# Performance work log

Hardware: AMD Instinct MI355X
Metric: run time of the kernel (lower is better)

The kernel has to match this reference:

```python
import jax, jax.numpy as jnp
import numpy as np

T, B, OBS, HID = 64, 1024, 8, 512
N_ODE_STEPS = 4  # fixed-step RK4 over t in [0, 1]
LN_EPS = 1e-5


def _ln(x, g, b):
    m = x.mean(-1, keepdims=True)
    v = ((x - m) ** 2).mean(-1, keepdims=True)
    return (x - m) / jnp.sqrt(v + LN_EPS) * g + b


def setup_inputs() -> dict:
    key = jax.random.key(0)
    ks = jax.random.split(key, 24)

    def w(k, shape, fan_in):
        s = 1.0 / np.sqrt(fan_in)
        return jax.random.uniform(k, shape, jnp.float32, -s, s)

    return {
        "xs": jax.random.normal(ks[0], (T, B, OBS), jnp.float32),
        # obs2hidden MLP: Linear + LayerNorm + LeakyReLU
        "obs_W": w(ks[1], (OBS, HID), OBS),
        "obs_b": w(ks[2], (HID,), OBS),
        "obs_ln_g": jnp.ones((HID,), jnp.float32),
        "obs_ln_b": jnp.zeros((HID,), jnp.float32),
        # ODE func MLP (time-concat input, 2 hidden layers, linear out)
        "ode_W1": w(ks[3], (HID + 1, HID), HID + 1),
        "ode_b1": w(ks[4], (HID,), HID + 1),
        "ode_ln1_g": jnp.ones((HID,), jnp.float32),
        "ode_ln1_b": jnp.zeros((HID,), jnp.float32),
        "ode_W2": w(ks[5], (HID, HID), HID),
        "ode_b2": w(ks[6], (HID,), HID),
        "ode_ln2_g": jnp.ones((HID,), jnp.float32),
        "ode_ln2_b": jnp.zeros((HID,), jnp.float32),
        "ode_Wout": w(ks[7], (HID, HID), HID),
        "ode_bout": w(ks[8], (HID,), HID),
        # GRU cell (torch gate order: r, z, n)
        "W_ih": w(ks[9], (HID, 3 * HID), HID),
        "b_ih": w(ks[10], (3 * HID,), HID),
        "W_hh": w(ks[11], (HID, 3 * HID), HID),
        "b_hh": w(ks[12], (3 * HID,), HID),
    }


def reference(xs, obs_W, obs_b, obs_ln_g, obs_ln_b,
              ode_W1, ode_b1, ode_ln1_g, ode_ln1_b,
              ode_W2, ode_b2, ode_ln2_g, ode_ln2_b,
              ode_Wout, ode_bout, W_ih, b_ih, W_hh, b_hh):
    batch = xs.shape[1]

    # obs -> hidden for all timesteps at once: [T, B, HID]
    hs = jax.nn.leaky_relu(_ln(xs @ obs_W + obs_b, obs_ln_g, obs_ln_b))

    def ode_f(h, t):  # h: [B, HID], t: scalar
        ht = jnp.concatenate([h, jnp.full((batch, 1), t, h.dtype)], axis=-1)
        z = jax.nn.leaky_relu(_ln(ht @ ode_W1 + ode_b1, ode_ln1_g, ode_ln1_b))
        z = jax.nn.leaky_relu(_ln(z @ ode_W2 + ode_b2, ode_ln2_g, ode_ln2_b))
        return z @ ode_Wout + ode_bout

    dt = 1.0 / N_ODE_STEPS

    def rk4_solve(h0):
        def body(h, t):
            k1 = ode_f(h, t)
            k2 = ode_f(h + 0.5 * dt * k1, t + 0.5 * dt)
            k3 = ode_f(h + 0.5 * dt * k2, t + 0.5 * dt)
            k4 = ode_f(h + dt * k3, t + dt)
            return h + (dt / 6.0) * (k1 + 2 * k2 + 2 * k3 + k4), None
        ts = jnp.arange(N_ODE_STEPS, dtype=h0.dtype) * dt
        h, _ = jax.lax.scan(body, h0, ts)
        return h

    def gru_cell(x, h):
        gi = x @ W_ih + b_ih
        gh = h @ W_hh + b_hh
        i_r, i_z, i_n = jnp.split(gi, 3, axis=-1)
        h_r, h_z, h_n = jnp.split(gh, 3, axis=-1)
        r = jax.nn.sigmoid(i_r + h_r)
        z = jax.nn.sigmoid(i_z + h_z)
        n = jnp.tanh(i_n + r * h_n)
        return (1.0 - z) * n + z * h

    def step(h_prev, h_obs):
        h_ode = rk4_solve(h_obs)          # NeuralODE: integrate from t=0 to 1
        h_new = gru_cell(h_ode, h_prev)   # GRU step
        return h_new, None

    h0 = jnp.zeros((batch, hs.shape[-1]), hs.dtype)
    h_final, _ = jax.lax.scan(step, h0, hs)
    return h_final  # [B, HID]
```

## Files before the change

kernel.cpp:

```cpp
#include <hip/hip_runtime.h>
#include <stdint.h>


typedef __bf16 bf16x8 __attribute__((ext_vector_type(8)));
typedef float floatx4 __attribute__((ext_vector_type(4)));

#define BP 40
#define KSP 516

static __device__ __forceinline__ float bf2f(unsigned short u) {
  union { unsigned int u32; float f; } c;
  c.u32 = ((unsigned int)u) << 16;
  return c.f;
}
static __device__ __forceinline__ unsigned short f2bf(float f) {
  union { __bf16 h; unsigned short u; } c;
  c.h = (__bf16)f;
  return c.u;
}
static __device__ __forceinline__ float lo_bf(unsigned int u) {
  union { unsigned int i; float f; } c; c.i = u << 16; return c.f;
}
static __device__ __forceinline__ float hi_bf(unsigned int u) {
  union { unsigned int i; float f; } c; c.i = u & 0xffff0000u; return c.f;
}
static __device__ __forceinline__ unsigned int pk2(float a, float b) {
  return (unsigned int)f2bf(a) | ((unsigned int)f2bf(b) << 16);
}

static __device__ __forceinline__ void barrier_lds() {
  __asm__ volatile("s_waitcnt lgkmcnt(0)\n\ts_barrier" ::: "memory");
}

static __device__ __forceinline__ float row16_sum(float v) {
  union { float f; int i; } c, d;
  c.f = v;
  d.i = __builtin_amdgcn_update_dpp(0, c.i, 0x111, 0xf, 0xf, true); c.f += d.f;
  d.i = __builtin_amdgcn_update_dpp(0, c.i, 0x112, 0xf, 0xf, true); c.f += d.f;
  d.i = __builtin_amdgcn_update_dpp(0, c.i, 0x114, 0xf, 0xf, true); c.f += d.f;
  d.i = __builtin_amdgcn_update_dpp(0, c.i, 0x118, 0xf, 0xf, true); c.f += d.f;
  return c.f;
}

__global__ void tile_weight(const float* __restrict__ src, unsigned short* __restrict__ dst) {
  int t = blockIdx.x * 256 + threadIdx.x;
  int ml = t & 15, qd = (t >> 4) & 3;
  int nt = (t >> 6) & 31, kk = t >> 11;
  int n = nt * 16 + ml;
  int k0 = kk * 32 + qd * 8;
  unsigned short o[8] __attribute__((aligned(16)));
#pragma unroll
  for (int j = 0; j < 8; ++j) o[j] = f2bf(src[(size_t)(k0 + j) * 512 + n]);
  *(uint4*)(dst + (size_t)t * 8) = *(const uint4*)o;
}

__global__ void transpose_f2b(const float* __restrict__ src, unsigned short* __restrict__ dst,
                              int R, int C) {
  __shared__ float t[32][33];
  int c0 = blockIdx.x * 32, r0 = blockIdx.y * 32;
  int tx = threadIdx.x, ty = threadIdx.y;
#pragma unroll
  for (int i = 0; i < 32; i += 8) t[ty + i][tx] = src[(size_t)(r0 + ty + i) * C + c0 + tx];
  __syncthreads();
#pragma unroll
  for (int i = 0; i < 32; i += 8) dst[(size_t)(c0 + ty + i) * R + r0 + tx] = f2bf(t[tx][ty + i]);
}

__global__ __launch_bounds__(256) void obs_embed(
    const float* __restrict__ xs, const float* __restrict__ W,
    const float* __restrict__ bias, const float* __restrict__ gam,
    const float* __restrict__ bet, unsigned short* __restrict__ Y) {
  __shared__ float Wl[4096];
  const int tid = threadIdx.x, lane = tid & 63, wv = tid >> 6;
#pragma unroll
  for (int i = 0; i < 16; ++i) Wl[i * 256 + tid] = W[i * 256 + tid];
  __syncthreads();
  size_t row = (size_t)blockIdx.x * 4 + wv;
  float xf[8];
  {
    const float* xp = xs + row * 8;
#pragma unroll
    for (int k = 0; k < 8; ++k) xf[k] = xp[k];
  }
  int n0 = lane * 8;
  float a[8];
#pragma unroll
  for (int j = 0; j < 8; ++j) a[j] = bias[n0 + j];
#pragma unroll
  for (int k = 0; k < 8; ++k)
#pragma unroll
    for (int j = 0; j < 8; ++j) a[j] += xf[k] * Wl[k * 512 + n0 + j];
  float s1 = 0.f, s2 = 0.f;
#pragma unroll
  for (int j = 0; j < 8; ++j) { s1 += a[j]; s2 += a[j] * a[j]; }
#pragma unroll
  for (int off = 1; off < 64; off <<= 1) { s1 += __shfl_xor(s1, off); s2 += __shfl_xor(s2, off); }
  float mean = s1 * (1.f / 512.f);
  float rstd = rsqrtf(s2 * (1.f / 512.f) - mean * mean + 1e-5f);
  unsigned short o[8] __attribute__((aligned(16)));
#pragma unroll
  for (int j = 0; j < 8; ++j) {
    float v = (a[j] - mean) * rstd * gam[n0 + j] + bet[n0 + j];
    v = v > 0.f ? v : 0.01f * v;
    o[j] = f2bf(v);
  }
  *(uint4*)(Y + row * 512 + n0) = *(const uint4*)o;
}


static __device__ __forceinline__ int a_addr(int row, int n) {
  return (((row >> 4) * 16 + (n >> 5)) * 4 + ((n >> 3) & 3)) * 128 + (row & 15) * 8 + (n & 7);
}

static __device__ __forceinline__ void bload(const unsigned short* __restrict__ Wt, int kk,
                                             int wvoff, bf16x8 (&b)[4]) {
  const unsigned short* p = Wt + (size_t)kk * 16384 + wvoff;
#pragma unroll
  for (int j = 0; j < 4; ++j) b[j] = *(const bf16x8*)(p + j * 512);
}

static __device__ __forceinline__ void gemmS(const unsigned short* __restrict__ Wt,
                                             const unsigned short* __restrict__ Wnext,
                                             const unsigned short* As, int wvoff, int lane,
                                             const float (&bias)[4],
                                             bf16x8 (&bb)[2][4], floatx4 (&acc)[4][4]) {
#pragma unroll
  for (int mi = 0; mi < 4; ++mi)
#pragma unroll
    for (int j = 0; j < 4; ++j)
      acc[mi][j] = (floatx4){bias[j], bias[j], bias[j], bias[j]};
#pragma unroll 2
  for (int kk = 0; kk < 16; ++kk) {
#pragma unroll
    for (int mh = 0; mh < 2; ++mh) {
      bf16x8 a0 = *(const bf16x8*)&As[((2 * mh) * 16 + kk) * 512 + lane * 8];
      bf16x8 a1 = *(const bf16x8*)&As[((2 * mh + 1) * 16 + kk) * 512 + lane * 8];
#pragma unroll
      for (int j = 0; j < 4; ++j) {
        acc[2 * mh][j] =
            __builtin_amdgcn_mfma_f32_16x16x32_bf16(a0, bb[kk & 1][j], acc[2 * mh][j], 0, 0, 0);
        acc[2 * mh + 1][j] =
            __builtin_amdgcn_mfma_f32_16x16x32_bf16(a1, bb[kk & 1][j], acc[2 * mh + 1][j], 0, 0, 0);
      }
    }
    if (kk < 14) bload(Wt, kk + 2, wvoff, bb[kk & 1]);
    else bload(Wnext, kk - 14, wvoff, bb[kk & 1]);
  }
}

static __device__ __forceinline__ void ln_epi(floatx4 (&acc)[4][4], unsigned short* As,
                                              const unsigned int* Psu, int wA, bool gmHi,
                                              int wB, bool btHi,
                                              int wv, int lane, int tid,
                                              float2* red, float* stat) {
  const int ml = lane & 15, qd = lane >> 4;
#pragma unroll
  for (int mi = 0; mi < 4; ++mi)
#pragma unroll
    for (int r = 0; r < 4; ++r) {
      float s1 = 0.f, s2 = 0.f;
#pragma unroll
      for (int j = 0; j < 4; ++j) { float x = acc[mi][j][r]; s1 += x; s2 += x * x; }
      s1 = row16_sum(s1);
      s2 = row16_sum(s2);
      if (ml == 15) red[(mi * 16 + 4 * qd + r) * 8 + wv] = make_float2(s1, s2);
    }
  barrier_lds();
  if (tid < 64) {
    float S1 = 0.f, S2 = 0.f;
#pragma unroll
    for (int w = 0; w < 8; ++w) { float2 v = red[tid * 8 + w]; S1 += v.x; S2 += v.y; }
    float mean = S1 * (1.f / 512.f);
    float var = S2 * (1.f / 512.f) - mean * mean;
    stat[tid * 2] = mean;
    stat[tid * 2 + 1] = rsqrtf(var + 1e-5f);
  }
  barrier_lds();
  float gm[4], bt[4];
#pragma unroll
  for (int j = 0; j < 4; ++j) {
    int n = (4 * wv + j) * 16 + ml;
    unsigned int a = Psu[wA * 512 + n];
    unsigned int b = Psu[wB * 512 + n];
    gm[j] = gmHi ? hi_bf(a) : lo_bf(a);
    bt[j] = btHi ? hi_bf(b) : lo_bf(b);
  }
#pragma unroll
  for (int mi = 0; mi < 4; ++mi) {
    float mean[4], rstd[4];
#pragma unroll
    for (int r = 0; r < 4; ++r) {
      int row = mi * 16 + 4 * qd + r;
      mean[r] = stat[row * 2];
      rstd[r] = stat[row * 2 + 1];
    }
#pragma unroll
    for (int j = 0; j < 4; ++j) {
      int n = (4 * wv + j) * 16 + ml;
#pragma unroll
      for (int r = 0; r < 4; ++r) {
        float x = (acc[mi][j][r] - mean[r]) * (rstd[r] * gm[j]) + bt[j];
        x = x > 0.f ? x : 0.01f * x;
        As[a_addr(mi * 16 + 4 * qd + r, n)] = f2bf(x);
      }
    }
  }
  barrier_lds();
}

static __device__ __forceinline__ void stage_epi(floatx4 (&acc)[4][4], float (&h)[4][4][4],
                                                 unsigned int* Ks, unsigned short* As,
                                                 unsigned short* Yb, size_t m0,
                                                 int stg, bool last, int wv, int lane) {
  const int ml = lane & 15, qd = lane >> 4;
  barrier_lds();
#pragma unroll
  for (int mi = 0; mi < 4; ++mi)
#pragma unroll
    for (int j = 0; j < 4; ++j) {
      int n = (4 * wv + j) * 16 + ml;
#pragma unroll
      for (int rp = 0; rp < 2; ++rp) {
        int kidx = (mi * 8 + qd * 2 + rp) * KSP + n;
        float kv0 = acc[mi][j][2 * rp];
        float kv1 = acc[mi][j][2 * rp + 1];
        unsigned int pk = (stg != 0) ? Ks[kidx] : 0u;
        float s0 = bf2f((unsigned short)(pk & 0xffffu));
        float s1 = bf2f((unsigned short)(pk >> 16));
        float h0 = h[mi][j][2 * rp], h1 = h[mi][j][2 * rp + 1];
        float y0, y1;
        if (stg == 0)      { s0 = kv0;        s1 = kv1;        y0 = h0 + 0.125f * kv0; y1 = h1 + 0.125f * kv1; }
        else if (stg == 1) { s0 += 2.f * kv0; s1 += 2.f * kv1; y0 = h0 + 0.125f * kv0; y1 = h1 + 0.125f * kv1; }
        else if (stg == 2) { s0 += 2.f * kv0; s1 += 2.f * kv1; y0 = h0 + 0.25f * kv0;  y1 = h1 + 0.25f * kv1; }
        else {
          h0 += (1.f / 24.f) * (s0 + kv0);
          h1 += (1.f / 24.f) * (s1 + kv1);
          h[mi][j][2 * rp] = h0; h[mi][j][2 * rp + 1] = h1;
          y0 = h0; y1 = h1;
        }
        if (stg != 3) Ks[kidx] = (unsigned int)f2bf(s0) | ((unsigned int)f2bf(s1) << 16);
        int row = mi * 16 + 4 * qd + 2 * rp;
        As[a_addr(row, n)] = f2bf(y0);
        As[a_addr(row + 1, n)] = f2bf(y1);
        if (last && stg == 3) {
          Yb[(m0 + row) * 512 + n] = f2bf(y0);
          Yb[(m0 + row + 1) * 512 + n] = f2bf(y1);
        }
      }
    }
  barrier_lds();
}

__global__ __launch_bounds__(512) void ode_mega(
    unsigned short* Yb, const unsigned short* __restrict__ W1t,
    const unsigned short* __restrict__ W2t, const unsigned short* __restrict__ Wot,
    const float* __restrict__ b1, const float* __restrict__ tr, const float* __restrict__ g1,
    const float* __restrict__ be1, const float* __restrict__ b2, const float* __restrict__ g2,
    const float* __restrict__ be2, const float* __restrict__ bo) {
  __shared__ __align__(16) unsigned short As[32768];
  __shared__ __align__(16) unsigned int Psu[2048];
  __shared__ float2 red[512];
  __shared__ float stat[128];
  __shared__ __align__(16) unsigned int Ks[32 * KSP];

  const int tid = threadIdx.x;
  const int lane = tid & 63;
  const int wv = tid >> 6;
  const int ml = lane & 15;
  const int qd = lane >> 4;
  const size_t m0 = (size_t)blockIdx.x * 64;
  const int wvoff = wv * 2048 + lane * 8;

  bf16x8 bb[2][4];
  bload(W1t, 0, wvoff, bb[0]);
  bload(W1t, 1, wvoff, bb[1]);

  Psu[0 * 512 + tid] = pk2(b1[tid], tr[tid]);
  Psu[1 * 512 + tid] = pk2(g1[tid], be1[tid]);
  Psu[2 * 512 + tid] = pk2(b2[tid], g2[tid]);
  Psu[3 * 512 + tid] = pk2(be2[tid], bo[tid]);

  {
    int r = tid >> 3;
    int c0 = tid & 7;
#pragma unroll
    for (int i = 0; i < 8; ++i) {
      int c = c0 + i * 8;
      uint4 v = *(const uint4*)(Yb + (m0 + r) * 512 + c * 8);
      int dst = (((r >> 4) * 16 + (c >> 2)) * 4 + (c & 3)) * 128 + (r & 15) * 8;
      *(uint4*)(As + dst) = v;
    }
  }
  barrier_lds();

  float h[4][4][4];
#pragma unroll
  for (int mi = 0; mi < 4; ++mi)
#pragma unroll
    for (int j = 0; j < 4; ++j) {
      int n = (4 * wv + j) * 16 + ml;
#pragma unroll
      for (int r = 0; r < 4; ++r) h[mi][j][r] = bf2f(As[a_addr(mi * 16 + 4 * qd + r, n)]);
    }

  for (int e = 0; e < 16; ++e) {
    int stg = e & 3;
    float tval = 0.25f * (float)(e >> 2) + ((stg == 3) ? 0.25f : (stg ? 0.125f : 0.f));
    floatx4 acc[4][4];
    float bias[4];

#pragma unroll
    for (int j = 0; j < 4; ++j) {
      unsigned int p0 = Psu[0 * 512 + (4 * wv + j) * 16 + ml];
      bias[j] = lo_bf(p0) + tval * hi_bf(p0);
    }
    gemmS(W1t, W2t, As, wvoff, lane, bias, bb, acc);
    ln_epi(acc, As, Psu, 1, false, 1, true, wv, lane, tid, red, stat);

#pragma unroll
    for (int j = 0; j < 4; ++j)
      bias[j] = lo_bf(Psu[2 * 512 + (4 * wv + j) * 16 + ml]);
    gemmS(W2t, Wot, As, wvoff, lane, bias, bb, acc);
    ln_epi(acc, As, Psu, 2, true, 3, false, wv, lane, tid, red, stat);

#pragma unroll
    for (int j = 0; j < 4; ++j)
      bias[j] = hi_bf(Psu[3 * 512 + (4 * wv + j) * 16 + ml]);
    gemmS(Wot, W1t, As, wvoff, lane, bias, bb, acc);
    stage_epi(acc, h, Ks, As, Yb, m0, stg, e == 15, wv, lane);
  }
}

__global__ __launch_bounds__(256) void gru_step(
    const unsigned short* __restrict__ Yt, const float* __restrict__ hprev,
    float* __restrict__ hnew, const unsigned short* __restrict__ Wiht,
    const unsigned short* __restrict__ Whht, const float* __restrict__ bih,
    const float* __restrict__ bhh) {
  __shared__ __align__(16) unsigned short Ay[32 * BP];
  __shared__ __align__(16) unsigned short Ah[32 * BP];
  __shared__ __align__(16) unsigned short Bg[6 * 64 * BP];
  const int tid = threadIdx.x, lane = tid & 63, wv = tid >> 6;
  const int ml = lane & 15, qd = lane >> 4;
  const int m0 = blockIdx.x * 32;
  const int j0 = blockIdx.y * 64;

  floatx4 acc[2][6];
#pragma unroll
  for (int mi = 0; mi < 2; ++mi)
#pragma unroll
    for (int g = 0; g < 6; ++g) acc[mi][g] = 0.f;

  for (int kk = 0; kk < 16; ++kk) {
    __syncthreads();
#pragma unroll
    for (int c = 0; c < 7; ++c) {
      int id = c * 256 + tid;
      if (id < 128) {
        int r = id >> 2, kc = id & 3;
        *(uint4*)(Ay + r * BP + kc * 8) =
            *(const uint4*)(Yt + (size_t)(m0 + r) * 512 + kk * 32 + kc * 8);
      } else if (id < 256) {
        int id2 = id - 128;
        int r = id2 >> 2, kc = id2 & 3;
        const float* s = hprev + (size_t)(m0 + r) * 512 + kk * 32 + kc * 8;
        unsigned short o[8] __attribute__((aligned(16)));
#pragma unroll
        for (int j = 0; j < 8; ++j) o[j] = f2bf(s[j]);
        *(uint4*)(Ah + r * BP + kc * 8) = *(const uint4*)o;
      } else {
        int id2 = id - 256;
        int g = id2 >> 8;
        int rem = id2 & 255;
        int r = rem >> 2, kc = rem & 3;
        const unsigned short* mat = (g < 3) ? Wiht : Whht;
        int gate = (g < 3) ? g : (g - 3);
        *(uint4*)(Bg + g * (64 * BP) + r * BP + kc * 8) =
            *(const uint4*)(mat + (size_t)(gate * 512 + j0 + r) * 512 + kk * 32 + kc * 8);
      }
    }
    __syncthreads();
    bf16x8 ay[2], ah[2];
#pragma unroll
    for (int mi = 0; mi < 2; ++mi) {
      ay[mi] = *(const bf16x8*)&Ay[(16 * mi + ml) * BP + qd * 8];
      ah[mi] = *(const bf16x8*)&Ah[(16 * mi + ml) * BP + qd * 8];
    }
#pragma unroll
    for (int g = 0; g < 6; ++g) {
      bf16x8 b = *(const bf16x8*)&Bg[g * (64 * BP) + (16 * wv + ml) * BP + qd * 8];
#pragma unroll
      for (int mi = 0; mi < 2; ++mi)
        acc[mi][g] = __builtin_amdgcn_mfma_f32_16x16x32_bf16((g < 3) ? ay[mi] : ah[mi], b,
                                                             acc[mi][g], 0, 0, 0);
    }
  }
  int j = j0 + 16 * wv + ml;
  float bi_r = bih[j], bi_z = bih[512 + j], bi_n = bih[1024 + j];
  float bh_r = bhh[j], bh_z = bhh[512 + j], bh_n = bhh[1024 + j];
#pragma unroll
  for (int mi = 0; mi < 2; ++mi)
#pragma unroll
    for (int r = 0; r < 4; ++r) {
      size_t row = (size_t)(m0 + 16 * mi + 4 * qd + r);
      float rg = acc[mi][0][r] + bi_r + acc[mi][3][r] + bh_r;
      rg = 1.f / (1.f + __expf(-rg));
      float zg = acc[mi][1][r] + bi_z + acc[mi][4][r] + bh_z;
      zg = 1.f / (1.f + __expf(-zg));
      float ng = tanhf(acc[mi][2][r] + bi_n + rg * (acc[mi][5][r] + bh_n));
      float hp = hprev[row * 512 + j];
      hnew[row * 512 + j] = (1.f - zg) * ng + zg * hp;
    }
}

__global__ void zero_h(float* hf) {
  int i = blockIdx.x * 256 + threadIdx.x;
  hf[i] = 0.f;
}

extern "C" void kernel_launch(void* const* d_in, const int* in_sizes, int n_in,
                              void* d_out, int out_size, void* d_ws, size_t ws_size,
                              hipStream_t stream) {
  (void)in_sizes; (void)n_in; (void)out_size; (void)ws_size;
  const float* xs    = (const float*)d_in[0];
  const float* obsW  = (const float*)d_in[1];
  const float* obsb  = (const float*)d_in[2];
  const float* obsg  = (const float*)d_in[3];
  const float* obsbe = (const float*)d_in[4];
  const float* W1    = (const float*)d_in[5];
  const float* b1    = (const float*)d_in[6];
  const float* g1    = (const float*)d_in[7];
  const float* be1   = (const float*)d_in[8];
  const float* W2    = (const float*)d_in[9];
  const float* b2    = (const float*)d_in[10];
  const float* g2    = (const float*)d_in[11];
  const float* be2   = (const float*)d_in[12];
  const float* Wo    = (const float*)d_in[13];
  const float* bo    = (const float*)d_in[14];
  const float* Wih   = (const float*)d_in[15];
  const float* bih   = (const float*)d_in[16];
  const float* Whh   = (const float*)d_in[17];
  const float* bhh   = (const float*)d_in[18];

  char* p = (char*)d_ws;
  auto take = [&](size_t bytes) { char* q = p; p += (bytes + 255) & ~(size_t)255; return q; };
  unsigned short* W1t  = (unsigned short*)take((size_t)512 * 512 * 2);
  unsigned short* W2t  = (unsigned short*)take((size_t)512 * 512 * 2);
  unsigned short* Wot  = (unsigned short*)take((size_t)512 * 512 * 2);
  unsigned short* Wiht = (unsigned short*)take((size_t)1536 * 512 * 2);
  unsigned short* Whht = (unsigned short*)take((size_t)1536 * 512 * 2);
  float* hf0 = (float*)take((size_t)1024 * 512 * 4);
  float* hf1 = (float*)take((size_t)1024 * 512 * 4);
  unsigned short* Yb = (unsigned short*)take((size_t)65536 * 512 * 2);

  dim3 tb(32, 8);
  tile_weight<<<128, 256, 0, stream>>>(W1, W1t);
  tile_weight<<<128, 256, 0, stream>>>(W2, W2t);
  tile_weight<<<128, 256, 0, stream>>>(Wo, Wot);
  transpose_f2b<<<dim3(48, 16), tb, 0, stream>>>(Wih, Wiht, 512, 1536);
  transpose_f2b<<<dim3(48, 16), tb, 0, stream>>>(Whh, Whht, 512, 1536);

  obs_embed<<<16384, 256, 0, stream>>>(xs, obsW, obsb, obsg, obsbe, Yb);

  ode_mega<<<1024, 512, 0, stream>>>(Yb, W1t, W2t, Wot, b1, W1 + 512 * 512, g1, be1, b2, g2,
                                     be2, bo);

  zero_h<<<2048, 256, 0, stream>>>(hf0);
  float* hf[2] = {hf0, hf1};
  for (int t = 0; t < 64; ++t) {
    int s = t & 1, d = s ^ 1;
    float* hn = (t == 63) ? (float*)d_out : hf[d];
    gru_step<<<dim3(32, 8), 256, 0, stream>>>(Yb + (size_t)t * 1024 * 512, hf[s], hn, Wiht, Whht,
                                              bih, bhh);
  }
}
```

Before: 3.391 ms.

## Swap MFMA operands so accumulators hold rows, simplify LayerNorm reduction

Swaps the A/B operands of the MFMA so each lane's accumulator holds four consecutive columns of a single row instead of four rows. LayerNorm statistics then need only two cross-quad shuffles and one barrier, and every wave computes mean/rstd itself instead of a second barrier and stats pass. Epilogue writes become packed 8-byte stores into the tiled LDS layout and to global memory. LN parameters are kept as fp32 in LDS with vector loads instead of packed bf16, which uses more shared memory and may reduce occupancy.

After: 3.280 ms. 1.03x faster.

```diff
diff --git a/kernel.cpp b/kernel.cpp
--- a/kernel.cpp
+++ b/kernel.cpp
@@ -6,7 +6,8 @@
 typedef float floatx4 __attribute__((ext_vector_type(4)));
 
 #define BP 40
-#define KSP 516
+#define KSR 257
+#define REDW 9
 
 static __device__ __forceinline__ float bf2f(unsigned short u) {
   union { unsigned int u32; float f; } c;
@@ -18,28 +19,12 @@
   c.h = (__bf16)f;
   return c.u;
 }
-static __device__ __forceinline__ float lo_bf(unsigned int u) {
-  union { unsigned int i; float f; } c; c.i = u << 16; return c.f;
-}
-static __device__ __forceinline__ float hi_bf(unsigned int u) {
-  union { unsigned int i; float f; } c; c.i = u & 0xffff0000u; return c.f;
-}
 static __device__ __forceinline__ unsigned int pk2(float a, float b) {
   return (unsigned int)f2bf(a) | ((unsigned int)f2bf(b) << 16);
 }
 
 static __device__ __forceinline__ void barrier_lds() {
   __asm__ volatile("s_waitcnt lgkmcnt(0)\n\ts_barrier" ::: "memory");
-}
-
-static __device__ __forceinline__ float row16_sum(float v) {
-  union { float f; int i; } c, d;
-  c.f = v;
-  d.i = __builtin_amdgcn_update_dpp(0, c.i, 0x111, 0xf, 0xf, true); c.f += d.f;
-  d.i = __builtin_amdgcn_update_dpp(0, c.i, 0x112, 0xf, 0xf, true); c.f += d.f;
-  d.i = __builtin_amdgcn_update_dpp(0, c.i, 0x114, 0xf, 0xf, true); c.f += d.f;
-  d.i = __builtin_amdgcn_update_dpp(0, c.i, 0x118, 0xf, 0xf, true); c.f += d.f;
-  return c.f;
 }
 
 __global__ void tile_weight(const float* __restrict__ src, unsigned short* __restrict__ dst) {
@@ -122,13 +107,12 @@
 static __device__ __forceinline__ void gemmS(const unsigned short* __restrict__ Wt,
                                              const unsigned short* __restrict__ Wnext,
                                              const unsigned short* As, int wvoff, int lane,
-                                             const float (&bias)[4],
+                                             const floatx4 (&bias)[4],
                                              bf16x8 (&bb)[2][4], floatx4 (&acc)[4][4]) {
 #pragma unroll
   for (int mi = 0; mi < 4; ++mi)
 #pragma unroll
-    for (int j = 0; j < 4; ++j)
-      acc[mi][j] = (floatx4){bias[j], bias[j], bias[j], bias[j]};
+    for (int j = 0; j < 4; ++j) acc[mi][j] = bias[j];
 #pragma unroll 2
   for (int kk = 0; kk < 16; ++kk) {
 #pragma unroll
@@ -138,9 +122,9 @@
 #pragma unroll
       for (int j = 0; j < 4; ++j) {
         acc[2 * mh][j] =
-            __builtin_amdgcn_mfma_f32_16x16x32_bf16(a0, bb[kk & 1][j], acc[2 * mh][j], 0, 0, 0);
+            __builtin_amdgcn_mfma_f32_16x16x32_bf16(bb[kk & 1][j], a0, acc[2 * mh][j], 0, 0, 0);
         acc[2 * mh + 1][j] =
-            __builtin_amdgcn_mfma_f32_16x16x32_bf16(a1, bb[kk & 1][j], acc[2 * mh + 1][j], 0, 0, 0);
+            __builtin_amdgcn_mfma_f32_16x16x32_bf16(bb[kk & 1][j], a1, acc[2 * mh + 1][j], 0, 0, 0);
       }
     }
     if (kk < 14) bload(Wt, kk + 2, wvoff, bb[kk & 1]);
@@ -149,60 +133,51 @@
 }
 
 static __device__ __forceinline__ void ln_epi(floatx4 (&acc)[4][4], unsigned short* As,
-                                              const unsigned int* Psu, int wA, bool gmHi,
-                                              int wB, bool btHi,
-                                              int wv, int lane, int tid,
-                                              float2* red, float* stat) {
+                                              const float* Pg, const float* Pb,
+                                              int wv, int lane, float2* red) {
   const int ml = lane & 15, qd = lane >> 4;
 #pragma unroll
-  for (int mi = 0; mi < 4; ++mi)
-#pragma unroll
-    for (int r = 0; r < 4; ++r) {
-      float s1 = 0.f, s2 = 0.f;
-#pragma unroll
-      for (int j = 0; j < 4; ++j) { float x = acc[mi][j][r]; s1 += x; s2 += x * x; }
-      s1 = row16_sum(s1);
-      s2 = row16_sum(s2);
-      if (ml == 15) red[(mi * 16 + 4 * qd + r) * 8 + wv] = make_float2(s1, s2);
-    }
+  for (int mi = 0; mi < 4; ++mi) {
+    float s1 = 0.f, s2 = 0.f;
+#pragma unroll
+    for (int j = 0; j < 4; ++j)
+#pragma unroll
+      for (int r = 0; r < 4; ++r) { float x = acc[mi][j][r]; s1 += x; s2 += x * x; }
+    s1 += __shfl_xor(s1, 16); s2 += __shfl_xor(s2, 16);
+    s1 += __shfl_xor(s1, 32); s2 += __shfl_xor(s2, 32);
+    if (qd == 0) red[(mi * 16 + ml) * REDW + wv] = make_float2(s1, s2);
+  }
   barrier_lds();
-  if (tid < 64) {
+  float mean[4], rstd[4];
+#pragma unroll
+  for (int mi = 0; mi < 4; ++mi) {
     float S1 = 0.f, S2 = 0.f;
 #pragma unroll
-    for (int w = 0; w < 8; ++w) { float2 v = red[tid * 8 + w]; S1 += v.x; S2 += v.y; }
-    float mean = S1 * (1.f / 512.f);
-    float var = S2 * (1.f / 512.f) - mean * mean;
-    stat[tid * 2] = mean;
-    stat[tid * 2 + 1] = rsqrtf(var + 1e-5f);
-  }
-  barrier_lds();
-  float gm[4], bt[4];
+    for (int w = 0; w < 8; ++w) {
+      float2 v = red[(mi * 16 + ml) * REDW + w];
+      S1 += v.x; S2 += v.y;
+    }
+    float m = S1 * (1.f / 512.f);
+    mean[mi] = m;
+    rstd[mi] = rsqrtf(S2 * (1.f / 512.f) - m * m + 1e-5f);
+  }
 #pragma unroll
   for (int j = 0; j < 4; ++j) {
-    int n = (4 * wv + j) * 16 + ml;
-    unsigned int a = Psu[wA * 512 + n];
-    unsigned int b = Psu[wB * 512 + n];
-    gm[j] = gmHi ? hi_bf(a) : lo_bf(a);
-    bt[j] = btHi ? hi_bf(b) : lo_bf(b);
-  }
-#pragma unroll
-  for (int mi = 0; mi < 4; ++mi) {
-    float mean[4], rstd[4];
-#pragma unroll
-    for (int r = 0; r < 4; ++r) {
-      int row = mi * 16 + 4 * qd + r;
-      mean[r] = stat[row * 2];
-      rstd[r] = stat[row * 2 + 1];
-    }
-#pragma unroll
-    for (int j = 0; j < 4; ++j) {
-      int n = (4 * wv + j) * 16 + ml;
-#pragma unroll
-      for (int r = 0; r < 4; ++r) {
-        float x = (acc[mi][j][r] - mean[r]) * (rstd[r] * gm[j]) + bt[j];
-        x = x > 0.f ? x : 0.01f * x;
-        As[a_addr(mi * 16 + 4 * qd + r, n)] = f2bf(x);
-      }
+    int nb = (4 * wv + j) * 16 + qd * 4;
+    floatx4 gm = *(const floatx4*)&Pg[nb];
+    floatx4 bt = *(const floatx4*)&Pb[nb];
+#pragma unroll
+    for (int mi = 0; mi < 4; ++mi) {
+      float x0 = (acc[mi][j][0] - mean[mi]) * rstd[mi] * gm[0] + bt[0];
+      float x1 = (acc[mi][j][1] - mean[mi]) * rstd[mi] * gm[1] + bt[1];
+      float x2 = (acc[mi][j][2] - mean[mi]) * rstd[mi] * gm[2] + bt[2];
+      float x3 = (acc[mi][j][3] - mean[mi]) * rstd[mi] * gm[3] + bt[3];
+      x0 = x0 > 0.f ? x0 : 0.01f * x0;
+      x1 = x1 > 0.f ? x1 : 0.01f * x1;
+      x2 = x2 > 0.f ? x2 : 0.01f * x2;
+      x3 = x3 > 0.f ? x3 : 0.01f * x3;
+      uint2 o = make_uint2(pk2(x0, x1), pk2(x2, x3));
+      *(uint2*)(As + a_addr(mi * 16 + ml, nb)) = o;
     }
   }
   barrier_lds();
@@ -215,19 +190,21 @@
   const int ml = lane & 15, qd = lane >> 4;
   barrier_lds();
 #pragma unroll
-  for (int mi = 0; mi < 4; ++mi)
+  for (int mi = 0; mi < 4; ++mi) {
+    int rowK = (mi * 16 + ml) * KSR;
 #pragma unroll
     for (int j = 0; j < 4; ++j) {
-      int n = (4 * wv + j) * 16 + ml;
-#pragma unroll
-      for (int rp = 0; rp < 2; ++rp) {
-        int kidx = (mi * 8 + qd * 2 + rp) * KSP + n;
-        float kv0 = acc[mi][j][2 * rp];
-        float kv1 = acc[mi][j][2 * rp + 1];
+      int nb = (4 * wv + j) * 16 + qd * 4;
+      unsigned int yw[2];
+#pragma unroll
+      for (int p = 0; p < 2; ++p) {
+        int kidx = rowK + (4 * wv + j) * 8 + qd * 2 + p;
+        float kv0 = acc[mi][j][2 * p];
+        float kv1 = acc[mi][j][2 * p + 1];
         unsigned int pk = (stg != 0) ? Ks[kidx] : 0u;
         float s0 = bf2f((unsigned short)(pk & 0xffffu));
         float s1 = bf2f((unsigned short)(pk >> 16));
-        float h0 = h[mi][j][2 * rp], h1 = h[mi][j][2 * rp + 1];
+        float h0 = h[mi][j][2 * p], h1 = h[mi][j][2 * p + 1];
         float y0, y1;
         if (stg == 0)      { s0 = kv0;        s1 = kv1;        y0 = h0 + 0.125f * kv0; y1 = h1 + 0.125f * kv1; }
         else if (stg == 1) { s0 += 2.f * kv0; s1 += 2.f * kv1; y0 = h0 + 0.125f * kv0; y1 = h1 + 0.125f * kv1; }
@@ -235,19 +212,18 @@
         else {
           h0 += (1.f / 24.f) * (s0 + kv0);
           h1 += (1.f / 24.f) * (s1 + kv1);
-          h[mi][j][2 * rp] = h0; h[mi][j][2 * rp + 1] = h1;
+          h[mi][j][2 * p] = h0; h[mi][j][2 * p + 1] = h1;
           y0 = h0; y1 = h1;
         }
-        if (stg != 3) Ks[kidx] = (unsigned int)f2bf(s0) | ((unsigned int)f2bf(s1) << 16);
-        int row = mi * 16 + 4 * qd + 2 * rp;
-        As[a_addr(row, n)] = f2bf(y0);
-        As[a_addr(row + 1, n)] = f2bf(y1);
-        if (last && stg == 3) {
-          Yb[(m0 + row) * 512 + n] = f2bf(y0);
-          Yb[(m0 + row + 1) * 512 + n] = f2bf(y1);
-        }
+        if (stg != 3) Ks[kidx] = pk2(s0, s1);
+        yw[p] = pk2(y0, y1);
       }
-    }
+      uint2 o = make_uint2(yw[0], yw[1]);
+      *(uint2*)(As + a_addr(mi * 16 + ml, nb)) = o;
+      if (last && stg == 3)
+        *(uint2*)(Yb + (m0 + mi * 16 + ml) * 512 + nb) = o;
+    }
+  }
   barrier_lds();
 }
 
@@ -258,10 +234,9 @@
     const float* __restrict__ be1, const float* __restrict__ b2, const float* __restrict__ g2,
     const float* __restrict__ be2, const float* __restrict__ bo) {
   __shared__ __align__(16) unsigned short As[32768];
-  __shared__ __align__(16) unsigned int Psu[2048];
-  __shared__ float2 red[512];
-  __shared__ float stat[128];
-  __shared__ __align__(16) unsigned int Ks[32 * KSP];
+  __shared__ __align__(16) float Pf[8 * 512];
+  __shared__ float2 red[64 * REDW];
+  __shared__ __align__(16) unsigned int Ks[64 * KSR];
 
   const int tid = threadIdx.x;
   const int lane = tid & 63;
@@ -275,10 +250,11 @@
   bload(W1t, 0, wvoff, bb[0]);
   bload(W1t, 1, wvoff, bb[1]);
 
-  Psu[0 * 512 + tid] = pk2(b1[tid], tr[tid]);
-  Psu[1 * 512 + tid] = pk2(g1[tid], be1[tid]);
-  Psu[2 * 512 + tid] = pk2(b2[tid], g2[tid]);
-  Psu[3 * 512 + tid] = pk2(be2[tid], bo[tid]);
+  {
+    const float* srcs[8] = {b1, tr, g1, be1, b2, g2, be2, bo};
+#pragma unroll
+    for (int v = 0; v < 8; ++v) Pf[v * 512 + tid] = srcs[v][tid];
+  }
 
   {
     int r = tid >> 3;
@@ -298,34 +274,44 @@
   for (int mi = 0; mi < 4; ++mi)
 #pragma unroll
     for (int j = 0; j < 4; ++j) {
-      int n = (4 * wv + j) * 16 + ml;
-#pragma unroll
-      for (int r = 0; r < 4; ++r) h[mi][j][r] = bf2f(As[a_addr(mi * 16 + 4 * qd + r, n)]);
+      int nb = (4 * wv + j) * 16 + qd * 4;
+      uint2 v = *(const uint2*)(As + a_addr(mi * 16 + ml, nb));
+      h[mi][j][0] = bf2f((unsigned short)(v.x & 0xffffu));
+      h[mi][j][1] = bf2f((unsigned short)(v.x >> 16));
+      h[mi][j][2] = bf2f((unsigned short)(v.y & 0xffffu));
+      h[mi][j][3] = bf2f((unsigned short)(v.y >> 16));
     }
 
   for (int e = 0; e < 16; ++e) {
     int stg = e & 3;
     float tval = 0.25f * (float)(e >> 2) + ((stg == 3) ? 0.25f : (stg ? 0.125f : 0.f));
     floatx4 acc[4][4];
-    float bias[4];
+    floatx4 bias[4];
 
 #pragma unroll
     for (int j = 0; j < 4; ++j) {
-      unsigned int p0 = Psu[0 * 512 + (4 * wv + j) * 16 + ml];
-      bias[j] = lo_bf(p0) + tval * hi_bf(p0);
+      int nb = (4 * wv + j) * 16 + qd * 4;
+      floatx4 vb = *(const floatx4*)&Pf[0 * 512 + nb];
+      floatx4 vt = *(const floatx4*)&Pf[1 * 512 + nb];
+#pragma unroll
+      for (int r = 0; r < 4; ++r) bias[j][r] = vb[r] + tval * vt[r];
     }
     gemmS(W1t, W2t, As, wvoff, lane, bias, bb, acc);
-    ln_epi(acc, As, Psu, 1, false, 1, true, wv, lane, tid, red, stat);
-
-#pragma unroll
-    for (int j = 0; j < 4; ++j)
-      bias[j] = lo_bf(Psu[2 * 512 + (4 * wv + j) * 16 + ml]);
+    ln_epi(acc, As, Pf + 2 * 512, Pf + 3 * 512, wv, lane, red);
+
+#pragma unroll
+    for (int j = 0; j < 4; ++j) {
+      int nb = (4 * wv + j) * 16 + qd * 4;
+      bias[j] = *(const floatx4*)&Pf[4 * 512 + nb];
+    }
     gemmS(W2t, Wot, As, wvoff, lane, bias, bb, acc);
-    ln_epi(acc, As, Psu, 2, true, 3, false, wv, lane, tid, red, stat);
-
-#pragma unroll
-    for (int j = 0; j < 4; ++j)
-      bias[j] = hi_bf(Psu[3 * 512 + (4 * wv + j) * 16 + ml]);
+    ln_epi(acc, As, Pf + 5 * 512, Pf + 6 * 512, wv, lane, red);
+
+#pragma unroll
+    for (int j = 0; j < 4; ++j) {
+      int nb = (4 * wv + j) * 16 + qd * 4;
+      bias[j] = *(const floatx4*)&Pf[7 * 512 + nb];
+    }
     gemmS(Wot, W1t, As, wvoff, lane, bias, bb, acc);
     stage_epi(acc, h, Ks, As, Yb, m0, stg, e == 15, wv, lane);
   }
```
